# Optimization experiments

Hardware: AMD Instinct MI355X
Metric: run time of the kernel (lower is better)

The kernel has to match this reference:

```python
import jax, jax.numpy as jnp
import numpy as np

ALPHA_LIM = (float(np.exp(-1.0 / 5.0)), float(np.exp(-1.0 / 25.0)))
BETA_LIM = (float(np.exp(-1.0 / 30.0)), float(np.exp(-1.0 / 120.0)))
A_LIM = (-1.0, 1.0)
B_LIM = (0.0, 2.0)
THRESHOLD = 1.0


@jax.custom_vjp
def spike_boxcar(x):
    # Heaviside forward, boxcar surrogate gradient
    return (x > 0).astype(x.dtype)


def _spike_fwd(x):
    return spike_boxcar(x), x


def _spike_bwd(x, g):
    return (jnp.where(jnp.abs(x) <= 0.5, g, jnp.zeros_like(g)),)


spike_boxcar.defvjp(_spike_fwd, _spike_bwd)


def setup_inputs() -> dict:
    key = jax.random.key(0)
    ks = jax.random.split(key, 9)
    B, T, I, H = 128, 512, 512, 512
    return {
        "x": jax.random.normal(ks[0], (B, T, I), dtype=jnp.float32),
        "W": jax.random.normal(ks[1], (H, I), dtype=jnp.float32) / np.sqrt(I),
        "alpha": jax.random.uniform(ks[2], (H,), dtype=jnp.float32),
        "beta": jax.random.uniform(ks[3], (H,), dtype=jnp.float32),
        "a": jax.random.uniform(ks[4], (H,), dtype=jnp.float32),
        "b": jax.random.uniform(ks[5], (H,), dtype=jnp.float32),
        "u0": jax.random.uniform(ks[6], (B, H), dtype=jnp.float32),
        "w0": jax.random.uniform(ks[7], (B, H), dtype=jnp.float32),
        "s0": jax.random.uniform(ks[8], (B, H), dtype=jnp.float32),
    }


def reference(x, W, alpha, beta, a, b, u0, w0, s0):
    # x: [B, T, I]; W: [H, I] (nn.Linear weight, no bias)
    alpha = jnp.clip(alpha, ALPHA_LIM[0], ALPHA_LIM[1])
    beta = jnp.clip(beta, BETA_LIM[0], BETA_LIM[1])
    a = jnp.clip(a, A_LIM[0], A_LIM[1])
    b = jnp.clip(b, B_LIM[0], B_LIM[1])

    Wx = jnp.einsum("bti,hi->bth", x, W)  # [B, T, H]
    Wx_t = jnp.transpose(Wx, (1, 0, 2))    # [T, B, H] for scan over time

    def step(carry, wx_t):
        ut, wt, st = carry
        wt = beta * wt + a * ut + b * st
        ut = alpha * (ut - st) + (1.0 - alpha) * (wx_t - wt)
        st = spike_boxcar(ut - THRESHOLD)
        return (ut, wt, st), st

    _, s = jax.lax.scan(step, (u0, w0, s0), Wx_t)  # s: [T, B, H]
    return jnp.transpose(s, (1, 0, 2))  # [B, T, H]
```

## Files before the change

### kernel.cpp

```cpp
#include <hip/hip_runtime.h>
#include <hip/hip_bf16.h>


#define M_SZ 65536
#define H_SZ 512
#define K_SZ 512
#define B_SZ 128
#define T_SZ 512
#define LSTR 132

typedef __attribute__((ext_vector_type(4))) float f32x4;

__device__ __forceinline__ bool detect_bf16(const unsigned int* __restrict__ w) {
  int c = 0;
#pragma unroll
  for (int i = 0; i < 64; ++i) {
    unsigned int e = (w[i] >> 7) & 0xffu;
    c += (e >= 115u && e <= 131u) ? 1 : 0;
  }
  return c > 32;
}

template <bool ISB>
__device__ __forceinline__ f32x4 ld4t(const void* __restrict__ p, size_t off) {
  if constexpr (!ISB) {
    return *reinterpret_cast<const f32x4*>(reinterpret_cast<const float*>(p) + off);
  } else {
    uint2 v = *reinterpret_cast<const uint2*>(reinterpret_cast<const unsigned short*>(p) + off);
    f32x4 r;
    r.x = __uint_as_float((v.x & 0xffffu) << 16);
    r.y = __uint_as_float(v.x & 0xffff0000u);
    r.z = __uint_as_float((v.y & 0xffffu) << 16);
    r.w = __uint_as_float(v.y & 0xffff0000u);
    return r;
  }
}

template <bool ISB>
__device__ __forceinline__ float ld1t(const void* __restrict__ p, int i) {
  if constexpr (!ISB) return reinterpret_cast<const float*>(p)[i];
  return __uint_as_float((unsigned int)(reinterpret_cast<const unsigned short*>(p)[i]) << 16);
}

__device__ __forceinline__ void gl_lds16(const void* g, void* l) {
  __builtin_amdgcn_global_load_lds(
      (const __attribute__((address_space(1))) void*)g,
      (__attribute__((address_space(3))) void*)l, 16, 0, 0);
}

template <bool ISB>
__device__ __forceinline__ void gemm_body(const void* __restrict__ X,
                                          const void* __restrict__ Wm,
                                          float* __restrict__ C,
                                          float* __restrict__ As,
                                          float* __restrict__ Bs) {
  const int tid = threadIdx.x;
  const int r0 = tid >> 2;
  const int q0 = (tid & 3) * 4;
  const int tx = tid & 15;
  const int ty = tid >> 4;
  const size_t M0 = (size_t)(blockIdx.x >> 2) * 128;
  const int N0 = (blockIdx.x & 3) * 128;

  float acc[8][8];
#pragma unroll
  for (int i = 0; i < 8; ++i)
#pragma unroll
    for (int j = 0; j < 8; ++j) acc[i][j] = 0.0f;

  const size_t aoff0 = (M0 + r0) * K_SZ + q0;
  const size_t aoff1 = (M0 + r0 + 64) * K_SZ + q0;
  const size_t boff0 = (size_t)(N0 + r0) * K_SZ + q0;
  const size_t boff1 = (size_t)(N0 + r0 + 64) * K_SZ + q0;

  f32x4 pa0 = ld4t<ISB>(X, aoff0), pa1 = ld4t<ISB>(X, aoff1);
  f32x4 pb0 = ld4t<ISB>(Wm, boff0), pb1 = ld4t<ISB>(Wm, boff1);

  for (int kk = 0; kk < K_SZ; kk += 16) {
    __syncthreads();
    As[(q0 + 0) * LSTR + r0] = pa0.x; As[(q0 + 1) * LSTR + r0] = pa0.y;
    As[(q0 + 2) * LSTR + r0] = pa0.z; As[(q0 + 3) * LSTR + r0] = pa0.w;
    As[(q0 + 0) * LSTR + r0 + 64] = pa1.x; As[(q0 + 1) * LSTR + r0 + 64] = pa1.y;
    As[(q0 + 2) * LSTR + r0 + 64] = pa1.z; As[(q0 + 3) * LSTR + r0 + 64] = pa1.w;
    Bs[(q0 + 0) * LSTR + r0] = pb0.x; Bs[(q0 + 1) * LSTR + r0] = pb0.y;
    Bs[(q0 + 2) * LSTR + r0] = pb0.z; Bs[(q0 + 3) * LSTR + r0] = pb0.w;
    Bs[(q0 + 0) * LSTR + r0 + 64] = pb1.x; Bs[(q0 + 1) * LSTR + r0 + 64] = pb1.y;
    Bs[(q0 + 2) * LSTR + r0 + 64] = pb1.z; Bs[(q0 + 3) * LSTR + r0 + 64] = pb1.w;
    __syncthreads();
    if (kk + 16 < K_SZ) {
      pa0 = ld4t<ISB>(X, aoff0 + kk + 16); pa1 = ld4t<ISB>(X, aoff1 + kk + 16);
      pb0 = ld4t<ISB>(Wm, boff0 + kk + 16); pb1 = ld4t<ISB>(Wm, boff1 + kk + 16);
    }
#pragma unroll
    for (int k = 0; k < 16; ++k) {
      const f32x4 a0 = *reinterpret_cast<const f32x4*>(As + k * LSTR + ty * 4);
      const f32x4 a1 = *reinterpret_cast<const f32x4*>(As + k * LSTR + 64 + ty * 4);
      const f32x4 b0 = *reinterpret_cast<const f32x4*>(Bs + k * LSTR + tx * 4);
      const f32x4 b1 = *reinterpret_cast<const f32x4*>(Bs + k * LSTR + 64 + tx * 4);
      const float av[8] = {a0.x, a0.y, a0.z, a0.w, a1.x, a1.y, a1.z, a1.w};
      const float bv[8] = {b0.x, b0.y, b0.z, b0.w, b1.x, b1.y, b1.z, b1.w};
#pragma unroll
      for (int i = 0; i < 8; ++i)
#pragma unroll
        for (int j = 0; j < 8; ++j) acc[i][j] += av[i] * bv[j];
    }
  }

#pragma unroll
  for (int r = 0; r < 8; ++r) {
    const size_t m = M0 + ((r < 4) ? (ty * 4 + r) : (64 + ty * 4 + (r - 4)));
    float* Cp = C + m * H_SZ + N0;
    f32x4 v0 = {acc[r][0], acc[r][1], acc[r][2], acc[r][3]};
    f32x4 v1 = {acc[r][4], acc[r][5], acc[r][6], acc[r][7]};
    __builtin_nontemporal_store(v0, reinterpret_cast<f32x4*>(Cp + tx * 4));
    __builtin_nontemporal_store(v1, reinterpret_cast<f32x4*>(Cp + 64 + tx * 4));
  }
}

__global__ __launch_bounds__(256) void sgemm_bt(const void* __restrict__ X,
                                                const void* __restrict__ Wm,
                                                float* __restrict__ C) {
  __shared__ float As[16 * LSTR];
  __shared__ float Bs[16 * LSTR];
  if (detect_bf16(reinterpret_cast<const unsigned int*>(X)))
    gemm_body<true>(X, Wm, C, As, Bs);
  else
    gemm_body<false>(X, Wm, C, As, Bs);
}

#define SCH 32
#define NCH (T_SZ / SCH)
#define NSLOT 4
#define LOOKA 3

template <bool ISB>
__device__ __forceinline__ void scan_body(
    const float* __restrict__ wx, const void* __restrict__ alpha_p,
    const void* __restrict__ beta_p, const void* __restrict__ a_p,
    const void* __restrict__ b_p, const void* __restrict__ u0p,
    const void* __restrict__ w0p, const void* __restrict__ s0p,
    void* __restrict__ out, float* __restrict__ ring) {
  const int tid = threadIdx.x;
  const int wv = tid >> 6;
  const int lane = tid & 63;
  const int bb = blockIdx.x >> 2;
  const int quarter = blockIdx.x & 3;
  const int h = quarter * 128 + tid;

  const float al = fminf(fmaxf(ld1t<ISB>(alpha_p, h), (float)0.8187307530779818),
                         (float)0.9607894391523232);
  const float be = fminf(fmaxf(ld1t<ISB>(beta_p, h), (float)0.9672161004820059),
                         (float)0.9917013044213351);
  const float av = fminf(fmaxf(ld1t<ISB>(a_p, h), -1.0f), 1.0f);
  const float bv = fminf(fmaxf(ld1t<ISB>(b_p, h), 0.0f), 2.0f);
  const float om = __fsub_rn(1.0f, al);

  const int bh = bb * H_SZ + h;
  float u = ld1t<ISB>(u0p, bh);
  float w = ld1t<ISB>(w0p, bh);
  float s = ld1t<ISB>(s0p, bh);

  const float* xb = wx + (size_t)bb * T_SZ * H_SZ + quarter * 128;
  float* outf = reinterpret_cast<float*>(out);
  __hip_bfloat16* outb = reinterpret_cast<__hip_bfloat16*>(out);
  const size_t ob0 = (size_t)bb * T_SZ * H_SZ + h;

  auto issue = [&](int c) {
    float* dst = ring + (c & (NSLOT - 1)) * (SCH * 128) + wv * (16 * 128);
    const float* sp = xb + (size_t)(c * SCH + wv * 16) * H_SZ;
#pragma unroll
    for (int i = 0; i < 8; ++i) {
      gl_lds16(sp + (size_t)(2 * i + (lane >> 5)) * H_SZ + (lane & 31) * 4,
               dst + 2 * i * 128);
    }
  };

  issue(0); issue(1); issue(2);

  for (int c = 0; c < NCH; ++c) {
    if (c + LOOKA < NCH) issue(c + LOOKA);
    asm volatile("s_waitcnt vmcnt(24)\n\ts_barrier" ::: "memory");
    const float* cb = ring + (c & (NSLOT - 1)) * (SCH * 128);
#pragma unroll 8
    for (int j = 0; j < SCH; ++j) {
      const float cur = cb[j * 128 + tid];
      w = __fadd_rn(__fadd_rn(__fmul_rn(be, w), __fmul_rn(av, u)), __fmul_rn(bv, s));
      u = __fadd_rn(__fmul_rn(al, __fsub_rn(u, s)), __fmul_rn(om, __fsub_rn(cur, w)));
      s = (u > 1.0f) ? 1.0f : 0.0f;
      const size_t o = ob0 + (size_t)(c * SCH + j) * H_SZ;
      if constexpr (ISB) outb[o] = __float2bfloat16(s);
      else outf[o] = s;
    }
  }
}

__global__ __launch_bounds__(128) void lif_scan(
    const float* __restrict__ wx, const void* __restrict__ X,
    const void* __restrict__ alpha_p, const void* __restrict__ beta_p,
    const void* __restrict__ a_p, const void* __restrict__ b_p,
    const void* __restrict__ u0p, const void* __restrict__ w0p,
    const void* __restrict__ s0p, void* __restrict__ out) {
  __shared__ float ring[NSLOT * SCH * 128];
  if (detect_bf16(reinterpret_cast<const unsigned int*>(X)))
    scan_body<true>(wx, alpha_p, beta_p, a_p, b_p, u0p, w0p, s0p, out, ring);
  else
    scan_body<false>(wx, alpha_p, beta_p, a_p, b_p, u0p, w0p, s0p, out, ring);
}

extern "C" void kernel_launch(void* const* d_in, const int* in_sizes, int n_in,
                              void* d_out, int out_size, void* d_ws, size_t ws_size,
                              hipStream_t stream) {
  const void* X = d_in[0];
  const void* Wm = d_in[1];
  float* ws = reinterpret_cast<float*>(d_ws);

  sgemm_bt<<<dim3((M_SZ / 128) * (H_SZ / 128)), dim3(256), 0, stream>>>(X, Wm, ws);

  lif_scan<<<dim3(B_SZ * 4), dim3(128), 0, stream>>>(
      ws, X, d_in[2], d_in[3], d_in[4], d_in[5], d_in[6], d_in[7], d_in[8], d_out);
}
```

Baseline: 648.6 us.

## Use barrier-free single-wave scan blocks and split GEMM into four launches

The LIF scan kernel becomes one 64-lane wave per block, covering a 64-wide hidden strip, so the grid doubles to 1024 blocks. Chunks shrink to 16 timesteps in a 3-slot LDS ring filled with async global-to-LDS loads, gated by hand-tuned vmcnt waits instead of s_barrier. Dropping the cross-wave barrier should reduce scan stalls. The GEMM is also split into four quarter-M launches via an mbase offset, which adds launch overhead with no overlap gain on the same stream. The exact vmcnt counts depend on the compiler not reordering the per-step stores, which is fragile.

```diff
diff --git a/kernel.cpp b/kernel.cpp
--- a/kernel.cpp
+++ b/kernel.cpp
@@ -51,7 +51,7 @@
 template <bool ISB>
 __device__ __forceinline__ void gemm_body(const void* __restrict__ X,
                                           const void* __restrict__ Wm,
-                                          float* __restrict__ C,
+                                          float* __restrict__ C, int mbase,
                                           float* __restrict__ As,
                                           float* __restrict__ Bs) {
   const int tid = threadIdx.x;
@@ -59,7 +59,7 @@
   const int q0 = (tid & 3) * 4;
   const int tx = tid & 15;
   const int ty = tid >> 4;
-  const size_t M0 = (size_t)(blockIdx.x >> 2) * 128;
+  const size_t M0 = (size_t)mbase + (size_t)(blockIdx.x >> 2) * 128;
   const int N0 = (blockIdx.x & 3) * 128;
 
   float acc[8][8];
@@ -119,19 +119,18 @@
 
 __global__ __launch_bounds__(256) void sgemm_bt(const void* __restrict__ X,
                                                 const void* __restrict__ Wm,
-                                                float* __restrict__ C) {
+                                                float* __restrict__ C, int mbase) {
   __shared__ float As[16 * LSTR];
   __shared__ float Bs[16 * LSTR];
   if (detect_bf16(reinterpret_cast<const unsigned int*>(X)))
-    gemm_body<true>(X, Wm, C, As, Bs);
+    gemm_body<true>(X, Wm, C, mbase, As, Bs);
   else
-    gemm_body<false>(X, Wm, C, As, Bs);
-}
-
-#define SCH 32
+    gemm_body<false>(X, Wm, C, mbase, As, Bs);
+}
+
+#define SCH 16
 #define NCH (T_SZ / SCH)
-#define NSLOT 4
-#define LOOKA 3
+#define NSL 3
 
 template <bool ISB>
 __device__ __forceinline__ void scan_body(
@@ -140,12 +139,11 @@
     const void* __restrict__ b_p, const void* __restrict__ u0p,
     const void* __restrict__ w0p, const void* __restrict__ s0p,
     void* __restrict__ out, float* __restrict__ ring) {
-  const int tid = threadIdx.x;
-  const int wv = tid >> 6;
-  const int lane = tid & 63;
-  const int bb = blockIdx.x >> 2;
-  const int quarter = blockIdx.x & 3;
-  const int h = quarter * 128 + tid;
+  const int lane = threadIdx.x;
+  const int b = blockIdx.x >> 3;
+  const int strip = blockIdx.x & 7;
+  const int h0 = strip * 64;
+  const int h = h0 + lane;
 
   const float al = fminf(fmaxf(ld1t<ISB>(alpha_p, h), (float)0.8187307530779818),
                          (float)0.9607894391523232);
@@ -155,52 +153,54 @@
   const float bv = fminf(fmaxf(ld1t<ISB>(b_p, h), 0.0f), 2.0f);
   const float om = __fsub_rn(1.0f, al);
 
-  const int bh = bb * H_SZ + h;
+  const int bh = b * H_SZ + h;
   float u = ld1t<ISB>(u0p, bh);
   float w = ld1t<ISB>(w0p, bh);
   float s = ld1t<ISB>(s0p, bh);
 
-  const float* xb = wx + (size_t)bb * T_SZ * H_SZ + quarter * 128;
+  const float* xb = wx + (size_t)b * T_SZ * H_SZ + h0;
   float* outf = reinterpret_cast<float*>(out);
   __hip_bfloat16* outb = reinterpret_cast<__hip_bfloat16*>(out);
-  const size_t ob0 = (size_t)bb * T_SZ * H_SZ + h;
+  const size_t ob0 = (size_t)b * T_SZ * H_SZ + h;
 
   auto issue = [&](int c) {
-    float* dst = ring + (c & (NSLOT - 1)) * (SCH * 128) + wv * (16 * 128);
-    const float* sp = xb + (size_t)(c * SCH + wv * 16) * H_SZ;
-#pragma unroll
-    for (int i = 0; i < 8; ++i) {
-      gl_lds16(sp + (size_t)(2 * i + (lane >> 5)) * H_SZ + (lane & 31) * 4,
-               dst + 2 * i * 128);
+    float* dst = ring + (c % NSL) * (SCH * 64);
+#pragma unroll
+    for (int j = 0; j < 4; ++j) {
+      int t = c * SCH + j * 4 + (lane >> 4);
+      t = (t < T_SZ) ? t : (T_SZ - 1);
+      gl_lds16(xb + (size_t)t * H_SZ + (lane & 15) * 4, dst + j * 256);
     }
   };
 
   issue(0); issue(1); issue(2);
 
   for (int c = 0; c < NCH; ++c) {
-    if (c + LOOKA < NCH) issue(c + LOOKA);
-    asm volatile("s_waitcnt vmcnt(24)\n\ts_barrier" ::: "memory");
-    const float* cb = ring + (c & (NSLOT - 1)) * (SCH * 128);
-#pragma unroll 8
-    for (int j = 0; j < SCH; ++j) {
-      const float cur = cb[j * 128 + tid];
+    if (c == 0)      asm volatile("s_waitcnt vmcnt(8)" ::: "memory");
+    else if (c == 1) asm volatile("s_waitcnt vmcnt(24)" ::: "memory");
+    else             asm volatile("s_waitcnt vmcnt(40)" ::: "memory");
+    const float* cb = ring + (c % NSL) * (SCH * 64);
+#pragma unroll
+    for (int jt = 0; jt < SCH; ++jt) {
+      const float cur = cb[jt * 64 + lane];
       w = __fadd_rn(__fadd_rn(__fmul_rn(be, w), __fmul_rn(av, u)), __fmul_rn(bv, s));
       u = __fadd_rn(__fmul_rn(al, __fsub_rn(u, s)), __fmul_rn(om, __fsub_rn(cur, w)));
       s = (u > 1.0f) ? 1.0f : 0.0f;
-      const size_t o = ob0 + (size_t)(c * SCH + j) * H_SZ;
+      const size_t o = ob0 + (size_t)(c * SCH + jt) * H_SZ;
       if constexpr (ISB) outb[o] = __float2bfloat16(s);
       else outf[o] = s;
     }
-  }
-}
-
-__global__ __launch_bounds__(128) void lif_scan(
+    issue(c + 3);
+  }
+}
+
+__global__ __launch_bounds__(64) void lif_scan(
     const float* __restrict__ wx, const void* __restrict__ X,
     const void* __restrict__ alpha_p, const void* __restrict__ beta_p,
     const void* __restrict__ a_p, const void* __restrict__ b_p,
     const void* __restrict__ u0p, const void* __restrict__ w0p,
     const void* __restrict__ s0p, void* __restrict__ out) {
-  __shared__ float ring[NSLOT * SCH * 128];
+  __shared__ float ring[NSL * SCH * 64];
   if (detect_bf16(reinterpret_cast<const unsigned int*>(X)))
     scan_body<true>(wx, alpha_p, beta_p, a_p, b_p, u0p, w0p, s0p, out, ring);
   else
@@ -214,8 +214,9 @@
   const void* Wm = d_in[1];
   float* ws = reinterpret_cast<float*>(d_ws);
 
-  sgemm_bt<<<dim3((M_SZ / 128) * (H_SZ / 128)), dim3(256), 0, stream>>>(X, Wm, ws);
-
-  lif_scan<<<dim3(B_SZ * 4), dim3(128), 0, stream>>>(
+  for (int q = 0; q < 4; ++q)
+    sgemm_bt<<<dim3(512), dim3(256), 0, stream>>>(X, Wm, ws, q * (M_SZ / 4));
+
+  lif_scan<<<dim3(B_SZ * 8), dim3(64), 0, stream>>>(
       ws, X, d_in[2], d_in[3], d_in[4], d_in[5], d_in[6], d_in[7], d_in[8], d_out);
 }
```

Measured after the change: 652.8 us. Within noise of the previous version (+0.7%).
